# Kernel tuning notes

Hardware: AMD Instinct MI355X
Metric: run time of the kernel (lower is better)

The kernel has to match this reference:

```python
import jax, jax.numpy as jnp
import numpy as np
from jax import lax

A = 3          # anchors per scale
C = 80         # num foreground classes (COCO)
NMS_THRESH = 0.45
NMS_TOPK = 400
POST_NMS = 100


def setup_inputs() -> dict:
    key = jax.random.key(0)
    k0, k1, k2 = jax.random.split(key, 3)
    B = 8
    ch = A * (C + 5)  # 255
    # raw head outputs (pre-decode conv activations), modest scale so exp() stays sane
    tip0 = jax.random.normal(k0, (B, ch, 19, 19), jnp.float32) * 0.5
    tip1 = jax.random.normal(k1, (B, ch, 38, 38), jnp.float32) * 0.5
    tip2 = jax.random.normal(k2, (B, ch, 76, 76), jnp.float32) * 0.5
    # standard YOLOv3 COCO anchors, deepest scale (stride 32) first
    anchors0 = jnp.array([[116., 90.], [156., 198.], [373., 326.]], jnp.float32)
    anchors1 = jnp.array([[30., 61.], [62., 45.], [59., 119.]], jnp.float32)
    anchors2 = jnp.array([[10., 13.], [16., 30.], [33., 23.]], jnp.float32)
    return dict(tip0=tip0, tip1=tip1, tip2=tip2,
                anchors0=anchors0, anchors1=anchors1, anchors2=anchors2)


def _decode(tip, anchors, stride):
    """YOLOOutputV3 inference decode. tip: (B, A*(C+5), H, W)."""
    B, _, H, W = tip.shape
    # (B, A*(C+5), H*W) -> (B, H*W, A, C+5)
    pred = tip.reshape(B, A * (C + 5), H * W).transpose(0, 2, 1).reshape(B, H * W, A, C + 5)
    gx, gy = jnp.meshgrid(jnp.arange(W), jnp.arange(H))       # each (H, W)
    offsets = jnp.stack([gx, gy], -1).reshape(1, H * W, 1, 2).astype(tip.dtype)
    centers = (jax.nn.sigmoid(pred[..., :2]) + offsets) * stride          # (B,HW,A,2)
    scales = jnp.exp(pred[..., 2:4]) * anchors.reshape(1, 1, A, 2)        # (B,HW,A,2)
    conf = jax.nn.sigmoid(pred[..., 4:5])                                 # objectness
    cls_scores = jax.nn.sigmoid(pred[..., 5:]) * conf                      # (B,HW,A,C)
    wh = scales * 0.5
    bbox = jnp.concatenate([centers - wh, centers + wh], -1)               # corner format
    return bbox.reshape(B, H * W * A, 4), cls_scores.reshape(B, H * W * A, C)


def _pairwise_iou(b):
    """b: (K,4) corner boxes -> (K,K) IoU."""
    x1, y1, x2, y2 = b[:, 0], b[:, 1], b[:, 2], b[:, 3]
    area = jnp.maximum(x2 - x1, 0.) * jnp.maximum(y2 - y1, 0.)
    iw = jnp.maximum(jnp.minimum(x2[:, None], x2[None, :]) - jnp.maximum(x1[:, None], x1[None, :]), 0.)
    ih = jnp.maximum(jnp.minimum(y2[:, None], y2[None, :]) - jnp.maximum(y1[:, None], y1[None, :]), 0.)
    inter = iw * ih
    return inter / (area[:, None] + area[None, :] - inter + 1e-12)


def _nms_single(det):
    """Class-aware greedy NMS on one image. det: (M,6) = (cid, score, x1,y1,x2,y2)."""
    K = NMS_TOPK
    _, idx = lax.top_k(det[:, 1], K)     # sort by score, keep top K
    d = det[idx]                          # (K,6), descending score
    iou = _pairwise_iou(d[:, 2:6])
    same = d[:, 0][:, None] == d[:, 0][None, :]   # only same class suppresses
    valid = d[:, 1] > 0.
    rng = jnp.arange(K)

    def body(i, keep):
        sup = (iou[i] > NMS_THRESH) & same[i] & (rng > i) & keep[i] & valid[i]
        return keep & ~sup

    keep = lax.fori_loop(0, K, body, jnp.ones((K,), bool)) & valid
    d = jnp.where(keep[:, None], d, jnp.full_like(d, -1.))
    order = jnp.argsort(-d[:, 1])         # kept (sorted) first, suppressed (-1) last
    return d[order][:POST_NMS]            # (POST_NMS, 6)


def _detect(tip0, tip1, tip2, anchors0, anchors1, anchors2):
    dets = []
    for tip, anc, stride in ((tip0, anchors0, 32), (tip1, anchors1, 16), (tip2, anchors2, 8)):
        bbox, scores = _decode(tip, anc, stride)          # (B,N,4), (B,N,C)
        B, N, _ = bbox.shape
        ids = jnp.broadcast_to(jnp.arange(C, dtype=bbox.dtype)[None, None, :, None], (B, N, C, 1))
        sc = scores[..., None]                            # (B,N,C,1)
        bx = jnp.broadcast_to(bbox[:, :, None, :], (B, N, C, 4))
        dets.append(jnp.concatenate([ids, sc, bx], -1).reshape(B, N * C, 6))
    det = jnp.concatenate(dets, 1)                        # (B, M, 6)
    return jax.vmap(_nms_single)(det)                     # (B, POST_NMS, 6)


def reference(tip0, tip1, tip2, anchors0, anchors1, anchors2):
    res = _detect(tip0, tip1, tip2, anchors0, anchors1, anchors2)
    ids = res[..., 0:1]
    scores = res[..., 1:2]
    bboxes = res[..., 2:6]
    return ids, scores, bboxes
```

## Files before the change

### kernel.cpp

```cpp
#include <hip/hip_runtime.h>
#include <stdint.h>

#define NUMA 3
#define NUMC 80
#define CAP  49152
#define KTOP 400
#define POST 100
#define EQCAP 1024
#define PFCAP 2048
#define KEY0 0x3EE66666u
#define KEYTOP 0x3F800000u
#define LBUF 1024
#define NMASK (KTOP * 7)

typedef float f32x4 __attribute__((ext_vector_type(4)));

__device__ __forceinline__ float sigmoidf_(float x) { return 1.0f / (1.0f + expf(-x)); }
__device__ __forceinline__ unsigned uminu(unsigned a, unsigned b) { return a < b ? a : b; }

__device__ __forceinline__ float thr_for(float cf) {
    if (!(cf >= 0.45f)) return 3.0e38f;
    float q = 0.449f / cf;
    float r = q / (1.0f - q);
    return logf(r) - 0.01f;
}

__global__ void init_kernel(unsigned* __restrict__ p) {
    int i = blockIdx.x * blockDim.x + threadIdx.x;
    if (i < 8) p[i] = 0;
}

__global__ __launch_bounds__(256) void score_main(
        const float* __restrict__ t0, const float* __restrict__ t1,
        const float* __restrict__ t2,
        unsigned* __restrict__ ccnt, unsigned* __restrict__ ckey,
        unsigned* __restrict__ cidx)
{
    __shared__ unsigned lkey[LBUF], lidx[LBUF];
    __shared__ unsigned lcnt, lbase;
    const int tid = threadIdx.x;
    if (tid == 0) lcnt = 0;
    __syncthreads();

    const int ba = blockIdx.z;
    const int b = ba / 3, a = ba - 3 * b;
    const int c0 = blockIdx.y * 10;
    const int cx = blockIdx.x;

    #define LEMIT(SC, IDX) do { \
        unsigned key_ = __float_as_uint(SC); \
        if (key_ >= KEY0) { \
            unsigned pos_ = atomicAdd(&lcnt, 1u); \
            if (pos_ < LBUF) { lkey[pos_] = key_; lidx[pos_] = (IDX); } \
        } \
    } while (0)

    if (cx < 2) {
        const int hw = cx * 256 + tid;
        if (hw < 361) {
            const float* base = t0 + (size_t)(b * 255 + a * 85) * 361;
            float cr = base[4 * 361 + hw];
            const float* p0 = base + (size_t)(5 + c0) * 361 + hw;
            float x0 = p0[0 * 361], x1 = p0[1 * 361], x2 = p0[2 * 361], x3 = p0[3 * 361];
            float x4 = p0[4 * 361], x5 = p0[5 * 361], x6 = p0[6 * 361], x7 = p0[7 * 361];
            float x8 = p0[8 * 361], x9 = p0[9 * 361];
            float cf = sigmoidf_(cr);
            float xt = thr_for(cf);
            unsigned ib = (unsigned)((hw * NUMA + a) * NUMC + c0);
            if (x0 > xt) LEMIT(sigmoidf_(x0) * cf, ib + 0);
            if (x1 > xt) LEMIT(sigmoidf_(x1) * cf, ib + 1);
            if (x2 > xt) LEMIT(sigmoidf_(x2) * cf, ib + 2);
            if (x3 > xt) LEMIT(sigmoidf_(x3) * cf, ib + 3);
            if (x4 > xt) LEMIT(sigmoidf_(x4) * cf, ib + 4);
            if (x5 > xt) LEMIT(sigmoidf_(x5) * cf, ib + 5);
            if (x6 > xt) LEMIT(sigmoidf_(x6) * cf, ib + 6);
            if (x7 > xt) LEMIT(sigmoidf_(x7) * cf, ib + 7);
            if (x8 > xt) LEMIT(sigmoidf_(x8) * cf, ib + 8);
            if (x9 > xt) LEMIT(sigmoidf_(x9) * cf, ib + 9);
        }
    } else {
        const float* tip; int vHW, v, candOff;
        if (cx < 4) { tip = t1; vHW = 361;  v = (cx - 2) * 256 + tid; candOff = 86640; }
        else        { tip = t2; vHW = 1444; v = (cx - 4) * 256 + tid; candOff = 433200; }
        if (v < vHW) {
            const f32x4* bp = (const f32x4*)(tip + (size_t)(b * 255 + a * 85) * (size_t)(vHW * 4));
            f32x4 cv = bp[(size_t)4 * vHW + v];
            const f32x4* p0 = bp + (size_t)(5 + c0) * vHW + v;
            f32x4 s0 = p0[0 * (size_t)vHW], s1 = p0[1 * (size_t)vHW];
            f32x4 s2 = p0[2 * (size_t)vHW], s3 = p0[3 * (size_t)vHW];
            f32x4 s4 = p0[4 * (size_t)vHW], s5 = p0[5 * (size_t)vHW];
            f32x4 s6 = p0[6 * (size_t)vHW], s7 = p0[7 * (size_t)vHW];
            f32x4 s8 = p0[8 * (size_t)vHW], s9 = p0[9 * (size_t)vHW];
            float cf0 = sigmoidf_(cv[0]), cf1 = sigmoidf_(cv[1]);
            float cf2 = sigmoidf_(cv[2]), cf3 = sigmoidf_(cv[3]);
            float xt0 = thr_for(cf0), xt1 = thr_for(cf1);
            float xt2 = thr_for(cf2), xt3 = thr_for(cf3);
            unsigned ib0 = (unsigned)(candOff + (v * 4 * NUMA + a) * NUMC + c0);
            #define EMIT4(S, U) do { \
                unsigned ib = ib0 + (U); \
                if ((S)[0] > xt0) LEMIT(sigmoidf_((S)[0]) * cf0, ib); \
                if ((S)[1] > xt1) LEMIT(sigmoidf_((S)[1]) * cf1, ib + 240); \
                if ((S)[2] > xt2) LEMIT(sigmoidf_((S)[2]) * cf2, ib + 480); \
                if ((S)[3] > xt3) LEMIT(sigmoidf_((S)[3]) * cf3, ib + 720); \
            } while (0)
            EMIT4(s0, 0); EMIT4(s1, 1); EMIT4(s2, 2); EMIT4(s3, 3);
            EMIT4(s4, 4); EMIT4(s5, 5); EMIT4(s6, 6); EMIT4(s7, 7);
            EMIT4(s8, 8); EMIT4(s9, 9);
            #undef EMIT4
        }
    }
    #undef LEMIT

    __syncthreads();
    if (tid == 0) {
        unsigned c = lcnt;
        if (c > LBUF) {
            atomicOr(&ccnt[b], 0x80000000u);
            lbase = 0xFFFFFFFFu;
        } else {
            lbase = atomicAdd(&ccnt[b], c);
        }
    }
    __syncthreads();
    unsigned c = uminu(lcnt, (unsigned)LBUF);
    unsigned basep = lbase;
    if (basep != 0xFFFFFFFFu) {
        for (unsigned i = tid; i < c; i += 256) {
            unsigned p = basep + i;
            if (p < CAP) {
                ckey[(size_t)b * CAP + p] = lkey[i];
                cidx[(size_t)b * CAP + p] = lidx[i];
            }
        }
    }
}

__device__ __forceinline__ void wave_select(const unsigned* h, int nbins, unsigned rank,
                                            unsigned* resv, int tid)
{
    if (tid >= 64) return;
    const int lane = tid;
    const int cs = nbins >> 6;
    unsigned v = 0;
    for (int k = 0; k < cs; k++) {
        int off = (k + lane) & (cs - 1);
        v += h[lane * cs + off];
    }
    unsigned S = v;
    #pragma unroll
    for (int o = 1; o < 64; o <<= 1) {
        unsigned t = (unsigned)__shfl_down((int)S, o);
        if (lane + o < 64) S += t;
    }
    unsigned long long bm = __ballot(S >= rank);
    if (bm == 0ull) bm = 1ull;
    int C = 63 - __builtin_clzll(bm);
    unsigned SC = (unsigned)__builtin_amdgcn_readlane((int)S, C);
    unsigned vC = (unsigned)__builtin_amdgcn_readlane((int)v, C);
    unsigned rem = rank - (SC - vC);
    unsigned w = (lane < cs) ? h[C * cs + lane] : 0u;
    unsigned T = w;
    #pragma unroll
    for (int o = 1; o < 64; o <<= 1) {
        unsigned t = (unsigned)__shfl_down((int)T, o);
        if (lane + o < 64) T += t;
    }
    unsigned long long bm2 = __ballot((T >= rem) && (lane < cs));
    if (bm2 == 0ull) bm2 = 1ull;
    int B = 63 - __builtin_clzll(bm2);
    unsigned TB = (unsigned)__builtin_amdgcn_readlane((int)T, B);
    unsigned wB = (unsigned)__builtin_amdgcn_readlane((int)w, B);
    if (lane == 0) {
        resv[0] = (unsigned)(C * cs + B);
        resv[1] = rem - (TB - wB);
    }
}

__global__ __launch_bounds__(1024) void topk_sel(
        const float* __restrict__ t0, const float* __restrict__ t1,
        const float* __restrict__ t2,
        const float* __restrict__ anc0, const float* __restrict__ anc1,
        const float* __restrict__ anc2,
        const unsigned* __restrict__ ccnt,
        unsigned* __restrict__ ckey, unsigned* __restrict__ cidx,
        float* __restrict__ dX1, float* __restrict__ dY1,
        float* __restrict__ dX2, float* __restrict__ dY2,
        float* __restrict__ dSC, unsigned* __restrict__ dCID)
{
    const int b = blockIdx.x;
    const int tid = threadIdx.x;
    const int T = 1024;

    __shared__ unsigned hist[4096];
    __shared__ unsigned resv[2];
    __shared__ unsigned selk[512], seli[512];
    __shared__ unsigned eqi[EQCAP];
    __shared__ unsigned pk[PFCAP], pi[PFCAP];
    __shared__ unsigned cnts[3];
    __shared__ unsigned fcnt;

    unsigned* ck = ckey + (size_t)b * CAP;
    unsigned* ci = cidx + (size_t)b * CAP;
    unsigned nraw = ccnt[b];
    unsigned kbase = KEY0;

    if (!(nraw >= KTOP && nraw <= CAP)) {
        const int NPOS = 3 * (361 + 1444 + 5776);
        for (int i = tid; i < 2048; i += T) hist[i] = 0;
        if (tid == 0) fcnt = 0;
        __syncthreads();
        for (int p = tid; p < NPOS; p += T) {
            const float* tip; int HW, pp;
            if (p < 1083)      { tip = t0; HW = 361;  pp = p; }
            else if (p < 5415) { tip = t1; HW = 1444; pp = p - 1083; }
            else               { tip = t2; HW = 5776; pp = p - 5415; }
            int a = pp / HW, hwl = pp - a * HW;
            const float* base = tip + (size_t)(b * 255 + a * 85) * HW;
            float cf = sigmoidf_(base[4 * HW + hwl]);
            for (int u = 0; u < NUMC; u++) {
                float sc = sigmoidf_(base[(size_t)(5 + u) * HW + hwl]) * cf;
                atomicAdd(&hist[__float_as_uint(sc) >> 19], 1u);
            }
        }
        __syncthreads();
        wave_select(hist, 2048, KTOP, resv, tid);
        __syncthreads();
        unsigned cutkey = resv[0] << 19;
        __syncthreads();
        for (int p = tid; p < NPOS; p += T) {
            const float* tip; int HW, pp, candOff;
            if (p < 1083)      { tip = t0; HW = 361;  pp = p;        candOff = 0; }
            else if (p < 5415) { tip = t1; HW = 1444; pp = p - 1083; candOff = 86640; }
            else               { tip = t2; HW = 5776; pp = p - 5415; candOff = 433200; }
            int a = pp / HW, hwl = pp - a * HW;
            const float* base = tip + (size_t)(b * 255 + a * 85) * HW;
            float cf = sigmoidf_(base[4 * HW + hwl]);
            unsigned ib0 = (unsigned)(candOff + (hwl * NUMA + a) * NUMC);
            for (int u = 0; u < NUMC; u++) {
                float sc = sigmoidf_(base[(size_t)(5 + u) * HW + hwl]) * cf;
                unsigned key = __float_as_uint(sc);
                if (key >= cutkey) {
                    unsigned pos = atomicAdd(&fcnt, 1u);
                    if (pos < CAP) { ck[pos] = key; ci[pos] = ib0 + (unsigned)u; }
                }
            }
        }
        __syncthreads();
        nraw = fcnt;
        kbase = cutkey;
    }
    unsigned n = uminu(nraw, (unsigned)CAP);

    unsigned span = (KEYTOP - kbase) + 1u;
    unsigned SH = 0;
    while ((span >> SH) > 2047u) SH++;

    for (int i = tid; i < 2048; i += T) hist[i] = 0;
    __syncthreads();
    {
        unsigned n4 = n >> 2;
        const uint4* ck4 = (const uint4*)ck;
        for (unsigned i = tid; i < n4; i += T) {
            uint4 k = ck4[i];
            atomicAdd(&hist[(k.x - kbase) >> SH], 1u);
            atomicAdd(&hist[(k.y - kbase) >> SH], 1u);
            atomicAdd(&hist[(k.z - kbase) >> SH], 1u);
            atomicAdd(&hist[(k.w - kbase) >> SH], 1u);
        }
        for (unsigned i = (n4 << 2) + tid; i < n; i += T)
            atomicAdd(&hist[(ck[i] - kbase) >> SH], 1u);
    }
    __syncthreads();
    wave_select(hist, 2048, KTOP, resv, tid);
    __syncthreads();
    unsigned Bf = resv[0];
    __syncthreads();

    if (tid == 0) { cnts[0] = 0; cnts[1] = 0; cnts[2] = 0; }
    __syncthreads();
    for (unsigned i = tid; i < n; i += T) {
        unsigned k = ck[i];
        if (((k - kbase) >> SH) >= Bf) {
            unsigned q = atomicAdd(&cnts[2], 1u);
            if (q < (unsigned)PFCAP) { pk[q] = k; pi[q] = ci[i]; }
        }
    }
    __syncthreads();
    unsigned pfCnt = cnts[2];
    bool useP = (pfCnt <= (unsigned)PFCAP);
    unsigned m = useP ? pfCnt : n;

    for (int i = tid; i < 4096; i += T) hist[i] = 0;
    __syncthreads();
    for (unsigned i = tid; i < m; i += T) {
        unsigned k = useP ? pk[i] : ck[i];
        atomicAdd(&hist[k >> 19], 1u);
    }
    __syncthreads();
    wave_select(hist, 4096, KTOP, resv, tid);
    __syncthreads();
    unsigned b1 = resv[0], r2 = resv[1];
    __syncthreads();

    for (int i = tid; i < 4096; i += T) hist[i] = 0;
    __syncthreads();
    for (unsigned i = tid; i < m; i += T) {
        unsigned k = useP ? pk[i] : ck[i];
        if ((k >> 19) == b1) atomicAdd(&hist[(k >> 7) & 0xFFFu], 1u);
    }
    __syncthreads();
    wave_select(hist, 4096, r2, resv, tid);
    __syncthreads();
    unsigned b2 = resv[0], r3 = resv[1];
    __syncthreads();

    for (int i = tid; i < 128; i += T) hist[i] = 0;
    __syncthreads();
    unsigned pref = (b1 << 12) | b2;
    for (unsigned i = tid; i < m; i += T) {
        unsigned k = useP ? pk[i] : ck[i];
        if ((k >> 7) == pref) atomicAdd(&hist[k & 127u], 1u);
    }
    __syncthreads();
    wave_select(hist, 128, r3, resv, tid);
    __syncthreads();
    unsigned b3 = resv[0], needEq = resv[1];
    unsigned K400 = (b1 << 19) | (b2 << 7) | b3;
    __syncthreads();

    for (int i = tid; i < 512; i += T) { selk[i] = 0u; seli[i] = 0xFFFFFFFFu; }
    for (int i = tid; i < EQCAP; i += T) eqi[i] = 0xFFFFFFFFu;
    __syncthreads();
    for (unsigned i = tid; i < m; i += T) {
        unsigned k = useP ? pk[i] : ck[i];
        if (k > K400) {
            unsigned idx = useP ? pi[i] : ci[i];
            unsigned p = atomicAdd(&cnts[0], 1u);
            if (p < 512u) { selk[p] = k; seli[p] = idx; }
        } else if (k == K400) {
            unsigned idx = useP ? pi[i] : ci[i];
            unsigned q = atomicAdd(&cnts[1], 1u);
            if (q < (unsigned)EQCAP) eqi[q] = idx;
        }
    }
    __syncthreads();
    unsigned selCnt = uminu(cnts[0], (unsigned)KTOP);
    unsigned eqN   = uminu(cnts[1], (unsigned)EQCAP);

    if (eqN > needEq) {
        int P2 = 1; while ((unsigned)P2 < eqN) P2 <<= 1;
        for (int k2 = 2; k2 <= P2; k2 <<= 1) {
            for (int j = k2 >> 1; j > 0; j >>= 1) {
                __syncthreads();
                for (int i = tid; i < P2; i += T) {
                    int ixj = i ^ j;
                    if (ixj > i && ixj < P2) {
                        unsigned va = eqi[i], vb = eqi[ixj];
                        bool up = ((i & k2) == 0);
                        if (up ? (va > vb) : (va < vb)) { eqi[i] = vb; eqi[ixj] = va; }
                    }
                }
            }
        }
        __syncthreads();
    }
    for (unsigned t2v = tid; t2v < needEq; t2v += T) {
        unsigned p = selCnt + t2v;
        if (p < KTOP) { selk[p] = K400; seli[p] = eqi[t2v]; }
    }
    __syncthreads();

    for (int k2 = 2; k2 <= 512; k2 <<= 1) {
        int j = k2 >> 1;
        for (; j >= 64; j >>= 1) {
            __syncthreads();
            if (tid < 512) {
                int i = tid, ixj = i ^ j;
                if (ixj > i) {
                    unsigned ka = selk[i], kb = selk[ixj], ia = seli[i], ib = seli[ixj];
                    bool before = (ka > kb) || (ka == kb && ia < ib);
                    bool up = ((i & k2) == 0);
                    if (up ? !before : before) {
                        selk[i] = kb; selk[ixj] = ka; seli[i] = ib; seli[ixj] = ia;
                    }
                }
            }
        }
        __syncthreads();
        if (tid < 512) {
            for (; j > 0; j >>= 1) {
                int i = tid, ixj = i ^ j;
                if (ixj > i) {
                    unsigned ka = selk[i], kb = selk[ixj], ia = seli[i], ib = seli[ixj];
                    bool before = (ka > kb) || (ka == kb && ia < ib);
                    bool up = ((i & k2) == 0);
                    if (up ? !before : before) {
                        selk[i] = kb; selk[ixj] = ka; seli[i] = ib; seli[ixj] = ia;
                    }
                }
            }
        }
    }
    __syncthreads();

    if (tid < KTOP) {
        unsigned idx = seli[tid];
        int o = b * KTOP + tid;
        if (idx == 0xFFFFFFFFu) {
            dX1[o] = -1.f; dY1[o] = -1.f; dX2[o] = -1.f; dY2[o] = -1.f;
            dSC[o] = __uint_as_float(selk[tid]); dCID[o] = 0u;
        } else {
            const float* tip; const float* anc; int HW, W, candOff; float strideF;
            if (idx < 86640u)       { tip = t0; anc = anc0; HW = 361;  W = 19; strideF = 32.f; candOff = 0; }
            else if (idx < 433200u) { tip = t1; anc = anc1; HW = 1444; W = 38; strideF = 16.f; candOff = 86640; }
            else                    { tip = t2; anc = anc2; HW = 5776; W = 76; strideF = 8.f;  candOff = 433200; }
            unsigned local = idx - (unsigned)candOff;
            int cls = (int)(local % NUMC);
            int nn  = (int)(local / NUMC);
            int a = nn % NUMA, hwl = nn / NUMA;
            const float* base = tip + (size_t)(b * 255 + a * 85) * HW + hwl;
            float tx = base[0];
            float ty = base[(size_t)HW];
            float tw = base[(size_t)2 * HW];
            float th = base[(size_t)3 * HW];
            float fx = (float)(hwl % W), fy = (float)(hwl / W);
            float cx = (sigmoidf_(tx) + fx) * strideF;
            float cy = (sigmoidf_(ty) + fy) * strideF;
            float hw_ = expf(tw) * anc[2 * a]     * 0.5f;
            float hh_ = expf(th) * anc[2 * a + 1] * 0.5f;
            dX1[o] = cx - hw_; dY1[o] = cy - hh_;
            dX2[o] = cx + hw_; dY2[o] = cy + hh_;
            dSC[o] = __uint_as_float(selk[tid]);
            dCID[o] = (unsigned)cls;
        }
    }
}

__global__ __launch_bounds__(1024) void nms_kernel(
        const float* __restrict__ dX1, const float* __restrict__ dY1,
        const float* __restrict__ dX2, const float* __restrict__ dY2,
        const float* __restrict__ dSC, const unsigned* __restrict__ dCID,
        float* __restrict__ out)
{
    __shared__ float lx1[KTOP], ly1[KTOP], lx2[KTOP], ly2[KTOP], lsc[KTOP];
    __shared__ int lcid[KTOP];
    __shared__ unsigned long long maskL[NMASK];
    __shared__ unsigned long long vkeep[7];
    __shared__ float oid[POST], osc[POST], obb[POST * 4];
    const int b = blockIdx.x;
    const int tid = threadIdx.x;

    for (int i = tid; i < KTOP; i += 1024) {
        int o = b * KTOP + i;
        lx1[i] = dX1[o]; ly1[i] = dY1[o];
        lx2[i] = dX2[o]; ly2[i] = dY2[o];
        lsc[i] = dSC[o]; lcid[i] = (int)dCID[o];
    }
    __syncthreads();

    for (int p = tid; p < NMASK; p += 1024) {
        int i = p / 7, w = p - i * 7;
        float x1i = lx1[i], y1i = ly1[i], x2i = lx2[i], y2i = ly2[i];
        float ai = fmaxf(x2i - x1i, 0.f) * fmaxf(y2i - y1i, 0.f);
        int cidI = lcid[i];
        unsigned long long m = 0ull;
        int j0 = w * 64;
        int rot = (9 * w) & 63;
        for (int t = 0; t < 64; t++) {
            int j = j0 + ((t + rot) & 63);
            if (j >= KTOP || j <= i) continue;
            if (lcid[j] != cidI) continue;
            float iw = fminf(x2i, lx2[j]) - fmaxf(x1i, lx1[j]);
            float ih = fminf(y2i, ly2[j]) - fmaxf(y1i, ly1[j]);
            iw = fmaxf(iw, 0.f); ih = fmaxf(ih, 0.f);
            float inter = iw * ih;
            float aj = fmaxf(lx2[j] - lx1[j], 0.f) * fmaxf(ly2[j] - ly1[j], 0.f);
            float iou = inter / (ai + aj - inter + 1e-12f);
            if (iou > 0.45f) m |= (1ull << (j - j0));
        }
        maskL[p] = m;
    }
    __syncthreads();

    if (tid < 64) {
        const int lane = tid;
        unsigned long long keep = 0ull;
        if (lane < 7) keep = (lane == 6) ? 0xFFFFull : ~0ull;
        unsigned long long mb[8];
        #pragma unroll
        for (int k = 0; k < 8; k++)
            mb[k] = (lane < 7) ? maskL[k * 7 + lane] : 0ull;
        for (int ib = 0; ib < KTOP; ib += 8) {
            #pragma unroll
            for (int k = 0; k < 8; k++) {
                int i = ib + k;
                unsigned long long m = mb[k];
                int nf = ib + 8 + k;
                mb[k] = (lane < 7 && nf < KTOP) ? maskL[nf * 7 + lane] : 0ull;
                int w = i >> 6;
                unsigned klo = (unsigned)__builtin_amdgcn_readlane((int)(unsigned)(keep & 0xFFFFFFFFull), w);
                unsigned khi = (unsigned)__builtin_amdgcn_readlane((int)(unsigned)(keep >> 32), w);
                unsigned long long kw = ((unsigned long long)khi << 32) | klo;
                if ((kw >> (i & 63)) & 1ull) keep &= ~m;
            }
        }
        if (lane < 7) vkeep[lane] = keep;
    } else {
        int q = tid - 64;
        if (q < POST) { oid[q] = -1.f; osc[q] = -1.f; }
        if (q < POST * 4) obb[q] = -1.f;
    }
    __syncthreads();

    if (tid < KTOP) {
        int w = tid >> 6, bp = tid & 63;
        unsigned long long kw = vkeep[w];
        if ((kw >> bp) & 1ull) {
            int r = 0;
            for (int q = 0; q < w; q++) r += __popcll(vkeep[q]);
            r += __popcll(kw & ((1ull << bp) - 1ull));
            if (r < POST) {
                oid[r] = (float)lcid[tid];
                osc[r] = lsc[tid];
                obb[r * 4 + 0] = lx1[tid];
                obb[r * 4 + 1] = ly1[tid];
                obb[r * 4 + 2] = lx2[tid];
                obb[r * 4 + 3] = ly2[tid];
            }
        }
    }
    __syncthreads();
    if (tid < POST) {
        out[b * POST + tid]       = oid[tid];
        out[800 + b * POST + tid] = osc[tid];
    }
    if (tid < POST * 4) out[1600 + b * POST * 4 + tid] = obb[tid];
}

extern "C" void kernel_launch(void* const* d_in, const int* in_sizes, int n_in,
                              void* d_out, int out_size, void* d_ws, size_t ws_size,
                              hipStream_t stream)
{
    const float* tip0 = (const float*)d_in[0];
    const float* tip1 = (const float*)d_in[1];
    const float* tip2 = (const float*)d_in[2];
    const float* anc0 = (const float*)d_in[3];
    const float* anc1 = (const float*)d_in[4];
    const float* anc2 = (const float*)d_in[5];
    float* out = (float*)d_out;

    unsigned* ccnt = (unsigned*)d_ws;
    unsigned* ckey = ccnt + 8;
    unsigned* cidx = ckey + (size_t)8 * CAP;
    float*    dX1  = (float*)(cidx + (size_t)8 * CAP);
    float*    dY1  = dX1 + 8 * KTOP;
    float*    dX2  = dY1 + 8 * KTOP;
    float*    dY2  = dX2 + 8 * KTOP;
    float*    dSC  = dY2 + 8 * KTOP;
    unsigned* dCID = (unsigned*)(dSC + 8 * KTOP);

    init_kernel<<<1, 64, 0, stream>>>(ccnt);

    dim3 g(10, 8, 24);
    score_main<<<g, 256, 0, stream>>>(tip0, tip1, tip2, ccnt, ckey, cidx);
    topk_sel<<<8, 1024, 0, stream>>>(tip0, tip1, tip2, anc0, anc1, anc2,
                                     ccnt, ckey, cidx,
                                     dX1, dY1, dX2, dY2, dSC, dCID);
    nms_kernel<<<8, 1024, 0, stream>>>(dX1, dY1, dX2, dY2, dSC, dCID, out);
}
```

Before: 200.8 us.

## Split NMS into parallel mask kernel and greedy kernel, widen score blocks

The IoU mask computation moves out of the single-block-per-batch NMS kernel into a separate kernel spread over many blocks per image, which writes masks to global memory. A lighter greedy kernel then reloads the masks and does the sequential suppression. The score kernel now handles 20 classes per block instead of 10, and the init kernel is replaced with hipMemsetAsync. This trades an extra launch and a global round trip of the masks for much more parallelism in the mask step. The wider score blocks also halve that grid and raise register pressure.

```diff
diff --git a/kernel.cpp b/kernel.cpp
--- a/kernel.cpp
+++ b/kernel.cpp
@@ -12,6 +12,7 @@
 #define KEYTOP 0x3F800000u
 #define LBUF 1024
 #define NMASK (KTOP * 7)
+#define CPB 20
 
 typedef float f32x4 __attribute__((ext_vector_type(4)));
 
@@ -23,11 +24,6 @@
     float q = 0.449f / cf;
     float r = q / (1.0f - q);
     return logf(r) - 0.01f;
-}
-
-__global__ void init_kernel(unsigned* __restrict__ p) {
-    int i = blockIdx.x * blockDim.x + threadIdx.x;
-    if (i < 8) p[i] = 0;
 }
 
 __global__ __launch_bounds__(256) void score_main(
@@ -44,7 +40,7 @@
 
     const int ba = blockIdx.z;
     const int b = ba / 3, a = ba - 3 * b;
-    const int c0 = blockIdx.y * 10;
+    const int c0 = blockIdx.y * CPB;
     const int cx = blockIdx.x;
 
     #define LEMIT(SC, IDX) do { \
@@ -61,22 +57,15 @@
             const float* base = t0 + (size_t)(b * 255 + a * 85) * 361;
             float cr = base[4 * 361 + hw];
             const float* p0 = base + (size_t)(5 + c0) * 361 + hw;
-            float x0 = p0[0 * 361], x1 = p0[1 * 361], x2 = p0[2 * 361], x3 = p0[3 * 361];
-            float x4 = p0[4 * 361], x5 = p0[5 * 361], x6 = p0[6 * 361], x7 = p0[7 * 361];
-            float x8 = p0[8 * 361], x9 = p0[9 * 361];
+            float xv[CPB];
+            #pragma unroll
+            for (int u = 0; u < CPB; u++) xv[u] = p0[u * 361];
             float cf = sigmoidf_(cr);
             float xt = thr_for(cf);
             unsigned ib = (unsigned)((hw * NUMA + a) * NUMC + c0);
-            if (x0 > xt) LEMIT(sigmoidf_(x0) * cf, ib + 0);
-            if (x1 > xt) LEMIT(sigmoidf_(x1) * cf, ib + 1);
-            if (x2 > xt) LEMIT(sigmoidf_(x2) * cf, ib + 2);
-            if (x3 > xt) LEMIT(sigmoidf_(x3) * cf, ib + 3);
-            if (x4 > xt) LEMIT(sigmoidf_(x4) * cf, ib + 4);
-            if (x5 > xt) LEMIT(sigmoidf_(x5) * cf, ib + 5);
-            if (x6 > xt) LEMIT(sigmoidf_(x6) * cf, ib + 6);
-            if (x7 > xt) LEMIT(sigmoidf_(x7) * cf, ib + 7);
-            if (x8 > xt) LEMIT(sigmoidf_(x8) * cf, ib + 8);
-            if (x9 > xt) LEMIT(sigmoidf_(x9) * cf, ib + 9);
+            #pragma unroll
+            for (int u = 0; u < CPB; u++)
+                if (xv[u] > xt) LEMIT(sigmoidf_(xv[u]) * cf, ib + (unsigned)u);
         }
     } else {
         const float* tip; int vHW, v, candOff;
@@ -86,27 +75,22 @@
             const f32x4* bp = (const f32x4*)(tip + (size_t)(b * 255 + a * 85) * (size_t)(vHW * 4));
             f32x4 cv = bp[(size_t)4 * vHW + v];
             const f32x4* p0 = bp + (size_t)(5 + c0) * vHW + v;
-            f32x4 s0 = p0[0 * (size_t)vHW], s1 = p0[1 * (size_t)vHW];
-            f32x4 s2 = p0[2 * (size_t)vHW], s3 = p0[3 * (size_t)vHW];
-            f32x4 s4 = p0[4 * (size_t)vHW], s5 = p0[5 * (size_t)vHW];
-            f32x4 s6 = p0[6 * (size_t)vHW], s7 = p0[7 * (size_t)vHW];
-            f32x4 s8 = p0[8 * (size_t)vHW], s9 = p0[9 * (size_t)vHW];
+            f32x4 sv[CPB];
+            #pragma unroll
+            for (int u = 0; u < CPB; u++) sv[u] = p0[(size_t)u * vHW];
             float cf0 = sigmoidf_(cv[0]), cf1 = sigmoidf_(cv[1]);
             float cf2 = sigmoidf_(cv[2]), cf3 = sigmoidf_(cv[3]);
             float xt0 = thr_for(cf0), xt1 = thr_for(cf1);
             float xt2 = thr_for(cf2), xt3 = thr_for(cf3);
             unsigned ib0 = (unsigned)(candOff + (v * 4 * NUMA + a) * NUMC + c0);
-            #define EMIT4(S, U) do { \
-                unsigned ib = ib0 + (U); \
-                if ((S)[0] > xt0) LEMIT(sigmoidf_((S)[0]) * cf0, ib); \
-                if ((S)[1] > xt1) LEMIT(sigmoidf_((S)[1]) * cf1, ib + 240); \
-                if ((S)[2] > xt2) LEMIT(sigmoidf_((S)[2]) * cf2, ib + 480); \
-                if ((S)[3] > xt3) LEMIT(sigmoidf_((S)[3]) * cf3, ib + 720); \
-            } while (0)
-            EMIT4(s0, 0); EMIT4(s1, 1); EMIT4(s2, 2); EMIT4(s3, 3);
-            EMIT4(s4, 4); EMIT4(s5, 5); EMIT4(s6, 6); EMIT4(s7, 7);
-            EMIT4(s8, 8); EMIT4(s9, 9);
-            #undef EMIT4
+            #pragma unroll
+            for (int u = 0; u < CPB; u++) {
+                unsigned ib = ib0 + (unsigned)u;
+                if (sv[u][0] > xt0) LEMIT(sigmoidf_(sv[u][0]) * cf0, ib);
+                if (sv[u][1] > xt1) LEMIT(sigmoidf_(sv[u][1]) * cf1, ib + 240);
+                if (sv[u][2] > xt2) LEMIT(sigmoidf_(sv[u][2]) * cf2, ib + 480);
+                if (sv[u][3] > xt3) LEMIT(sigmoidf_(sv[u][3]) * cf3, ib + 720);
+            }
         }
     }
     #undef LEMIT
@@ -436,29 +420,24 @@
     }
 }
 
-__global__ __launch_bounds__(1024) void nms_kernel(
+__global__ __launch_bounds__(256) void mask_kernel(
         const float* __restrict__ dX1, const float* __restrict__ dY1,
         const float* __restrict__ dX2, const float* __restrict__ dY2,
-        const float* __restrict__ dSC, const unsigned* __restrict__ dCID,
-        float* __restrict__ out)
+        const unsigned* __restrict__ dCID, unsigned long long* __restrict__ maskG)
 {
-    __shared__ float lx1[KTOP], ly1[KTOP], lx2[KTOP], ly2[KTOP], lsc[KTOP];
+    __shared__ float lx1[KTOP], ly1[KTOP], lx2[KTOP], ly2[KTOP];
     __shared__ int lcid[KTOP];
-    __shared__ unsigned long long maskL[NMASK];
-    __shared__ unsigned long long vkeep[7];
-    __shared__ float oid[POST], osc[POST], obb[POST * 4];
-    const int b = blockIdx.x;
+    const int b = blockIdx.y;
     const int tid = threadIdx.x;
-
-    for (int i = tid; i < KTOP; i += 1024) {
+    for (int i = tid; i < KTOP; i += 256) {
         int o = b * KTOP + i;
         lx1[i] = dX1[o]; ly1[i] = dY1[o];
         lx2[i] = dX2[o]; ly2[i] = dY2[o];
-        lsc[i] = dSC[o]; lcid[i] = (int)dCID[o];
-    }
-    __syncthreads();
-
-    for (int p = tid; p < NMASK; p += 1024) {
+        lcid[i] = (int)dCID[o];
+    }
+    __syncthreads();
+    int p = blockIdx.x * 256 + tid;
+    if (p < NMASK) {
         int i = p / 7, w = p - i * 7;
         float x1i = lx1[i], y1i = ly1[i], x2i = lx2[i], y2i = ly2[i];
         float ai = fmaxf(x2i - x1i, 0.f) * fmaxf(y2i - y1i, 0.f);
@@ -478,8 +457,25 @@
             float iou = inter / (ai + aj - inter + 1e-12f);
             if (iou > 0.45f) m |= (1ull << (j - j0));
         }
-        maskL[p] = m;
-    }
+        maskG[(size_t)b * NMASK + p] = m;
+    }
+}
+
+__global__ __launch_bounds__(512) void greedy_kernel(
+        const float* __restrict__ dX1, const float* __restrict__ dY1,
+        const float* __restrict__ dX2, const float* __restrict__ dY2,
+        const float* __restrict__ dSC, const unsigned* __restrict__ dCID,
+        const unsigned long long* __restrict__ maskG, float* __restrict__ out)
+{
+    __shared__ unsigned long long maskL[NMASK];
+    __shared__ unsigned long long vkeep[7];
+    __shared__ float oid[POST], osc[POST], obb[POST * 4];
+    const int b = blockIdx.x;
+    const int tid = threadIdx.x;
+
+    for (int i = tid; i < NMASK; i += 512) maskL[i] = maskG[(size_t)b * NMASK + i];
+    if (tid < POST) { oid[tid] = -1.f; osc[tid] = -1.f; }
+    if (tid < POST * 4) obb[tid] = -1.f;
     __syncthreads();
 
     if (tid < 64) {
@@ -505,10 +501,6 @@
             }
         }
         if (lane < 7) vkeep[lane] = keep;
-    } else {
-        int q = tid - 64;
-        if (q < POST) { oid[q] = -1.f; osc[q] = -1.f; }
-        if (q < POST * 4) obb[q] = -1.f;
     }
     __syncthreads();
 
@@ -520,12 +512,13 @@
             for (int q = 0; q < w; q++) r += __popcll(vkeep[q]);
             r += __popcll(kw & ((1ull << bp) - 1ull));
             if (r < POST) {
-                oid[r] = (float)lcid[tid];
-                osc[r] = lsc[tid];
-                obb[r * 4 + 0] = lx1[tid];
-                obb[r * 4 + 1] = ly1[tid];
-                obb[r * 4 + 2] = lx2[tid];
-                obb[r * 4 + 3] = ly2[tid];
+                int o = b * KTOP + tid;
+                oid[r] = (float)(int)dCID[o];
+                osc[r] = dSC[o];
+                obb[r * 4 + 0] = dX1[o];
+                obb[r * 4 + 1] = dY1[o];
+                obb[r * 4 + 2] = dX2[o];
+                obb[r * 4 + 3] = dY2[o];
             }
         }
     }
@@ -558,13 +551,16 @@
     float*    dY2  = dX2 + 8 * KTOP;
     float*    dSC  = dY2 + 8 * KTOP;
     unsigned* dCID = (unsigned*)(dSC + 8 * KTOP);
-
-    init_kernel<<<1, 64, 0, stream>>>(ccnt);
-
-    dim3 g(10, 8, 24);
+    unsigned long long* maskG = (unsigned long long*)(dCID + 8 * KTOP);
+
+    hipMemsetAsync(ccnt, 0, 8 * sizeof(unsigned), stream);
+
+    dim3 g(10, 80 / CPB, 24);
     score_main<<<g, 256, 0, stream>>>(tip0, tip1, tip2, ccnt, ckey, cidx);
     topk_sel<<<8, 1024, 0, stream>>>(tip0, tip1, tip2, anc0, anc1, anc2,
                                      ccnt, ckey, cidx,
                                      dX1, dY1, dX2, dY2, dSC, dCID);
-    nms_kernel<<<8, 1024, 0, stream>>>(dX1, dY1, dX2, dY2, dSC, dCID, out);
-}
+    mask_kernel<<<dim3((NMASK + 255) / 256, 8), 256, 0, stream>>>(
+        dX1, dY1, dX2, dY2, dCID, maskG);
+    greedy_kernel<<<8, 512, 0, stream>>>(dX1, dY1, dX2, dY2, dSC, dCID, maskG, out);
+}
```

After: 189.5 us. 5.7% less time.
